# Kernel optimization log

Measured on AMD Instinct MI355X. Metric: run time of the kernel, lower is better.

Reference implementation:

```python
import jax, jax.numpy as jnp
import numpy as np
import math

D_MODEL = 128
NHEAD = 8


def setup_inputs() -> dict:
    key = jax.random.key(0)
    k1, k2 = jax.random.split(key)
    x = jax.random.normal(k1, (1, 128, 64, 64), dtype=jnp.float32)
    # Conv2d(in_c=128, out=3*d_model=384, kernel 1x1, bias=False) -> (384, 128)
    W_qkv = jax.random.normal(k2, (384, 128), dtype=jnp.float32) * (1.0 / math.sqrt(128))
    return {"x": x, "W_qkv": W_qkv}


def reference(x, W_qkv):
    b, c, h, w = x.shape
    n = h * w
    d_head = D_MODEL // NHEAD
    # 1x1 conv == channel-wise linear projection
    qkv = jnp.einsum('bchw,oc->bohw', x, W_qkv)          # (b, 3*d_model, h, w)
    # flatten(2).reshape(b, nhead, -1, h*w).permute(0,1,3,2)
    t = qkv.reshape(b, NHEAD, 3 * d_head, n)
    t = jnp.transpose(t, (0, 1, 3, 2))                   # (b, nhead, n, 3*d_head)
    q, k, v = jnp.split(t, 3, axis=-1)                   # each (b, nhead, n, d_head)
    # NOTE: original scales by sqrt(d_model), not sqrt(d_head)
    scale = 1.0 / math.sqrt(D_MODEL)
    scores = jnp.einsum('bhnd,bhmd->bhnm', q * scale, k)  # (b, nhead, n, n)
    attn = jax.nn.softmax(scores, axis=-1)
    out = jnp.einsum('bhnm,bhmd->bhnd', attn, v)         # (b, nhead, n, d_head)
    out = jnp.transpose(out, (0, 1, 3, 2)).reshape(b, D_MODEL, h, w)
    return out
```

## Files before the change

kernel.cpp:

```cpp
#include <hip/hip_runtime.h>
#include <hip/hip_bf16.h>


typedef __attribute__((ext_vector_type(4))) float    f32x4;
typedef __attribute__((ext_vector_type(8))) short    s16x8;
typedef __attribute__((ext_vector_type(4))) short    s16x4;
typedef __attribute__((ext_vector_type(8))) __bf16   bf16x8;
typedef __attribute__((ext_vector_type(4))) unsigned u32x4;

union FragAB { s16x8 s; bf16x8 b; u32x4 u; };

__device__ __forceinline__ short f2bf(float f) {
    unsigned u = __float_as_uint(f);
    u += 0x7fff + ((u >> 16) & 1);
    return (short)(u >> 16);
}

__device__ __forceinline__ unsigned pkbf(float a, float b) {
    float2 f2; f2.x = a; f2.y = b;
    __hip_bfloat162 h = __float22bfloat162_rn(f2);
    unsigned r;
    __builtin_memcpy(&r, &h, 4);
    return r;
}

#if __has_builtin(__builtin_amdgcn_exp2f)
  #define FASTEXP(x) __builtin_amdgcn_exp2f(x)
  #define QK_SCALE 0.12751744154070513f
#else
  #define FASTEXP(x) __expf(x)
  #define QK_SCALE 0.08838834764831845f
#endif

__global__ __launch_bounds__(256) void qkv_kernel(
    const float* __restrict__ x, const float* __restrict__ w,
    short* __restrict__ qT, short* __restrict__ kv)
{
    __shared__ __align__(16) short xT[4][16][136];
    const int wv   = threadIdx.x >> 6;
    const int lane = threadIdx.x & 63;
    const int colL = lane & 15, quad = lane >> 4;
    const int n0 = blockIdx.x * 64 + wv * 16;
    const int oq = blockIdx.y;

    #pragma unroll
    for (int rr = 0; rr < 4; ++rr) {
        int c  = rr * 32 + (lane >> 1);
        int nh = (lane & 1) * 8;
        f32x4 a = *(const f32x4*)&x[c * 4096 + n0 + nh];
        f32x4 b = *(const f32x4*)&x[c * 4096 + n0 + nh + 4];
        #pragma unroll
        for (int t = 0; t < 4; ++t) {
            xT[wv][nh + t][c]     = f2bf(a[t]);
            xT[wv][nh + 4 + t][c] = f2bf(b[t]);
        }
    }
    __syncthreads();

    FragAB xb[4];
    #pragma unroll
    for (int ks = 0; ks < 4; ++ks)
        xb[ks].s = *(const s16x8*)&xT[wv][colL][ks * 32 + quad * 8];

    const int T    = blockIdx.x;
    const int wloc = wv * 16 + colL;
    const int cc   = wloc >> 5;
    const int bb   = (wloc >> 4) & 1;
    const int qp   = (wloc >> 2) & 3;
    const int jj   = bb * 4 + (wloc & 3);

    #pragma unroll
    for (int i = 0; i < 6; ++i) {
        const int otg  = oq * 6 + i;
        const int ob   = otg * 16;
        const int h    = otg / 3;
        const int kind = otg % 3;
        f32x4 acc = {0.f, 0.f, 0.f, 0.f};
        #pragma unroll
        for (int ks = 0; ks < 4; ++ks) {
            f32x4 wa0 = *(const f32x4*)&w[(ob + colL) * 128 + ks * 32 + quad * 8];
            f32x4 wa1 = *(const f32x4*)&w[(ob + colL) * 128 + ks * 32 + quad * 8 + 4];
            FragAB wa;
            #pragma unroll
            for (int t = 0; t < 4; ++t) {
                wa.s[t]     = f2bf(wa0[t]);
                wa.s[t + 4] = f2bf(wa1[t]);
            }
            acc = __builtin_amdgcn_mfma_f32_16x16x32_bf16(wa.b, xb[ks].b, acc, 0, 0, 0);
        }
        if (kind == 0) {
            s16x4 pk;
            #pragma unroll
            for (int r = 0; r < 4; ++r) pk[r] = f2bf(acc[r] * QK_SCALE);
            *(s16x4*)&qT[(h * 4096 + n0 + colL) * 16 + quad * 4] = pk;
        } else if (kind == 1) {
            s16x4 pk;
            #pragma unroll
            for (int r = 0; r < 4; ++r) pk[r] = f2bf(acc[r]);
            *(s16x4*)&kv[(h * 64 + T) * 2048 + wloc * 16 + quad * 4] = pk;
        } else {
            #pragma unroll
            for (int r = 0; r < 4; ++r) {
                int d = quad * 4 + r;
                kv[(h * 64 + T) * 2048 + 1024 + d * 64 + cc * 32 + qp * 8 + jj] = f2bf(acc[r]);
            }
        }
    }
}

template<int SPLIT>
__global__ __launch_bounds__(256) void attn_kernel(
    const short* __restrict__ qT, const short* __restrict__ kv,
    float* __restrict__ Opart, float* __restrict__ lpart,
    float* __restrict__ out)
{
    const int wv   = threadIdx.x >> 6;
    const int lane = threadIdx.x & 63;
    const int colL = lane & 15, quad = lane >> 4;

    const int bx = blockIdx.x;
    int s, h, b;
    if (SPLIT > 1) { s = bx >> 7; h = (bx >> 4) & 7; b = bx & 15; }
    else           { s = 0;       h = bx >> 4;       b = bx & 15; }
    const int qbase = b * 256 + wv * 64;
    const int nkt = 64 / SPLIT;

    FragAB qfs[4];
    #pragma unroll
    for (int u = 0; u < 4; ++u) {
        qfs[u].s = 0;
        if (quad < 2)
            qfs[u].s = *(const s16x8*)&qT[(h * 4096 + qbase + u * 16 + colL) * 16 + quad * 8];
    }

    FragAB ones;
    #pragma unroll
    for (int j = 0; j < 8; ++j) ones.s[j] = (short)0x3F80;

    f32x4 o[4], ol[4];
    #pragma unroll
    for (int u = 0; u < 4; ++u) {
        o[u]  = (f32x4){0.f, 0.f, 0.f, 0.f};
        ol[u] = (f32x4){0.f, 0.f, 0.f, 0.f};
    }

    const int voffK = colL * 16 + quad * 8;
    const int voffV = 1024 + colL * 64 + quad * 8;

    const short* kvb = kv + (h * 64 + s * nkt) * 2048;

    #pragma unroll
    for (int kt = 0; kt < nkt; ++kt) {
        FragAB kf[4], vf[2];
        #pragma unroll
        for (int t = 0; t < 4; ++t)
            kf[t].s = *(const s16x8*)&kvb[voffK + t * 256];
        #pragma unroll
        for (int c = 0; c < 2; ++c)
            vf[c].s = *(const s16x8*)&kvb[voffV + c * 32];
        kvb += 2048;

        #pragma unroll
        for (int u = 0; u < 4; ++u) {
            f32x4 st[4];
            #pragma unroll
            for (int t = 0; t < 4; ++t) {
                f32x4 z = {0.f, 0.f, 0.f, 0.f};
                st[t] = __builtin_amdgcn_mfma_f32_16x16x32_bf16(kf[t].b, qfs[u].b, z, 0, 0, 0);
            }
            FragAB p0, p1;
            #pragma unroll
            for (int t = 0; t < 2; ++t) {
                p0.u[t * 2 + 0] = pkbf(FASTEXP(st[t][0]), FASTEXP(st[t][1]));
                p0.u[t * 2 + 1] = pkbf(FASTEXP(st[t][2]), FASTEXP(st[t][3]));
                p1.u[t * 2 + 0] = pkbf(FASTEXP(st[t + 2][0]), FASTEXP(st[t + 2][1]));
                p1.u[t * 2 + 1] = pkbf(FASTEXP(st[t + 2][2]), FASTEXP(st[t + 2][3]));
            }
            o[u]  = __builtin_amdgcn_mfma_f32_16x16x32_bf16(vf[0].b, p0.b, o[u],  0, 0, 0);
            ol[u] = __builtin_amdgcn_mfma_f32_16x16x32_bf16(ones.b,  p0.b, ol[u], 0, 0, 0);
            o[u]  = __builtin_amdgcn_mfma_f32_16x16x32_bf16(vf[1].b, p1.b, o[u],  0, 0, 0);
            ol[u] = __builtin_amdgcn_mfma_f32_16x16x32_bf16(ones.b,  p1.b, ol[u], 0, 0, 0);
        }
    }

    #pragma unroll
    for (int u = 0; u < 4; ++u) {
        const float l = ol[u][0];
        const int q0 = qbase + u * 16;
        if (SPLIT > 1) {
            #pragma unroll
            for (int r = 0; r < 4; ++r)
                Opart[((s * 8 + h) * 16 + quad * 4 + r) * 4096 + q0 + colL] = o[u][r];
            if (quad == 0) lpart[(s * 8 + h) * 4096 + q0 + colL] = l;
        } else {
            const float inv = 1.f / l;
            #pragma unroll
            for (int r = 0; r < 4; ++r)
                out[(h * 16 + quad * 4 + r) * 4096 + q0 + colL] = o[u][r] * inv;
        }
    }
}

template<int SPLIT>
__global__ __launch_bounds__(256) void combine_kernel(
    const float* __restrict__ Opart, const float* __restrict__ lpart,
    float* __restrict__ out)
{
    const int row = blockIdx.x >> 2;
    const int n   = (blockIdx.x & 3) * 1024 + threadIdx.x * 4;
    const int h   = row >> 4;
    f32x4 osum = {0.f, 0.f, 0.f, 0.f}, lsum = {0.f, 0.f, 0.f, 0.f};
    #pragma unroll
    for (int s = 0; s < SPLIT; ++s) {
        osum += *(const f32x4*)&Opart[(s * 128 + row) * 4096 + n];
        lsum += *(const f32x4*)&lpart[(s * 8 + h) * 4096 + n];
    }
    f32x4 res;
    #pragma unroll
    for (int r = 0; r < 4; ++r) res[r] = osum[r] / lsum[r];
    *(f32x4*)&out[row * 4096 + n] = res;
}

extern "C" void kernel_launch(void* const* d_in, const int* in_sizes, int n_in,
                              void* d_out, int out_size, void* d_ws, size_t ws_size,
                              hipStream_t stream) {
    const float* x = (const float*)d_in[0];
    const float* w = (const float*)d_in[1];
    float* out = (float*)d_out;

    char* ws = (char*)d_ws;
    short* qT = (short*)ws;
    short* kv = (short*)(ws + (1u << 20));

    constexpr int SPLIT = 8;
    const size_t opart_bytes = (size_t)SPLIT * 128 * 4096 * 4;
    const size_t lpart_bytes = (size_t)SPLIT * 8 * 4096 * 4;
    const size_t need_split  = (3ull << 20) + opart_bytes + lpart_bytes;

    dim3 gq(64, 4);
    qkv_kernel<<<gq, 256, 0, stream>>>(x, w, qT, kv);

    if (ws_size >= need_split) {
        float* Opart = (float*)(ws + (3ull << 20));
        float* lpart = (float*)(ws + (3ull << 20) + opart_bytes);
        attn_kernel<SPLIT><<<SPLIT * 128, 256, 0, stream>>>(qT, kv, Opart, lpart, out);
        combine_kernel<SPLIT><<<512, 256, 0, stream>>>(Opart, lpart, out);
    } else {
        attn_kernel<1><<<128, 256, 0, stream>>>(qT, kv, nullptr, nullptr, out);
    }
}
```

Before: 97.16 us.

## Split keys across waves in-block and combine via LDS, dropping combine kernel

Replaces the grid-level split-K attention, which wrote partial O and l to global memory and reduced them in a separate combine kernel, with 512-thread blocks. Each of the 8 waves in a block handles one eighth of the keys for the same 64 queries, and the partials are reduced through shared memory. This removes the global partial-result traffic and one kernel launch. It also uses the 16x16x16 bf16 MFMA for QK^T when available, so the 16-wide head dimension is no longer zero-padded to 32. The costs are a block-wide sync and higher register and LDS pressure per block.

Measured after the change: 86.37 us. -11.1%, faster.

```diff
diff --git a/kernel.cpp b/kernel.cpp
--- a/kernel.cpp
+++ b/kernel.cpp
@@ -30,6 +30,12 @@
 #else
   #define FASTEXP(x) __expf(x)
   #define QK_SCALE 0.08838834764831845f
+#endif
+
+#if __has_builtin(__builtin_amdgcn_mfma_f32_16x16x16bf16_1k)
+  #define HAVE_MFMA16 1
+#else
+  #define HAVE_MFMA16 0
 #endif
 
 __global__ __launch_bounds__(256) void qkv_kernel(
@@ -108,23 +114,27 @@
     }
 }
 
-template<int SPLIT>
-__global__ __launch_bounds__(256) void attn_kernel(
+__global__ __launch_bounds__(512, 4) void attn_kernel(
     const short* __restrict__ qT, const short* __restrict__ kv,
-    float* __restrict__ Opart, float* __restrict__ lpart,
     float* __restrict__ out)
 {
+    __shared__ float lds_o[8][16][66];
+    __shared__ float lds_l[8][64];
+
     const int wv   = threadIdx.x >> 6;
     const int lane = threadIdx.x & 63;
     const int colL = lane & 15, quad = lane >> 4;
 
-    const int bx = blockIdx.x;
-    int s, h, b;
-    if (SPLIT > 1) { s = bx >> 7; h = (bx >> 4) & 7; b = bx & 15; }
-    else           { s = 0;       h = bx >> 4;       b = bx & 15; }
-    const int qbase = b * 256 + wv * 64;
-    const int nkt = 64 / SPLIT;
-
+    const int h     = blockIdx.x >> 6;
+    const int qb    = blockIdx.x & 63;
+    const int qbase = qb * 64;
+
+#if HAVE_MFMA16
+    s16x4 qfs[4];
+    #pragma unroll
+    for (int u = 0; u < 4; ++u)
+        qfs[u] = *(const s16x4*)&qT[(h * 4096 + qbase + u * 16 + colL) * 16 + quad * 4];
+#else
     FragAB qfs[4];
     #pragma unroll
     for (int u = 0; u < 4; ++u) {
@@ -132,6 +142,7 @@
         if (quad < 2)
             qfs[u].s = *(const s16x8*)&qT[(h * 4096 + qbase + u * 16 + colL) * 16 + quad * 8];
     }
+#endif
 
     FragAB ones;
     #pragma unroll
@@ -144,17 +155,27 @@
         ol[u] = (f32x4){0.f, 0.f, 0.f, 0.f};
     }
 
-    const int voffK = colL * 16 + quad * 8;
-    const int voffV = 1024 + colL * 64 + quad * 8;
-
-    const short* kvb = kv + (h * 64 + s * nkt) * 2048;
-
-    #pragma unroll
-    for (int kt = 0; kt < nkt; ++kt) {
-        FragAB kf[4], vf[2];
+    const int voffK16 = colL * 16 + quad * 4;
+    const int voffK32 = colL * 16 + quad * 8;
+    const int voffV   = 1024 + colL * 64 + quad * 8;
+    (void)voffK32; (void)voffK16;
+
+    const short* kvb = kv + (h * 64 + wv * 8) * 2048;
+
+    #pragma unroll
+    for (int kt = 0; kt < 8; ++kt) {
+#if HAVE_MFMA16
+        s16x4 kf[4];
         #pragma unroll
         for (int t = 0; t < 4; ++t)
-            kf[t].s = *(const s16x8*)&kvb[voffK + t * 256];
+            kf[t] = *(const s16x4*)&kvb[voffK16 + t * 256];
+#else
+        FragAB kf[4];
+        #pragma unroll
+        for (int t = 0; t < 4; ++t)
+            kf[t].s = *(const s16x8*)&kvb[voffK32 + t * 256];
+#endif
+        FragAB vf[2];
         #pragma unroll
         for (int c = 0; c < 2; ++c)
             vf[c].s = *(const s16x8*)&kvb[voffV + c * 32];
@@ -166,7 +187,11 @@
             #pragma unroll
             for (int t = 0; t < 4; ++t) {
                 f32x4 z = {0.f, 0.f, 0.f, 0.f};
+#if HAVE_MFMA16
+                st[t] = __builtin_amdgcn_mfma_f32_16x16x16bf16_1k(kf[t], qfs[u], z, 0, 0, 0);
+#else
                 st[t] = __builtin_amdgcn_mfma_f32_16x16x32_bf16(kf[t].b, qfs[u].b, z, 0, 0, 0);
+#endif
             }
             FragAB p0, p1;
             #pragma unroll
@@ -185,40 +210,31 @@
 
     #pragma unroll
     for (int u = 0; u < 4; ++u) {
-        const float l = ol[u][0];
-        const int q0 = qbase + u * 16;
-        if (SPLIT > 1) {
-            #pragma unroll
-            for (int r = 0; r < 4; ++r)
-                Opart[((s * 8 + h) * 16 + quad * 4 + r) * 4096 + q0 + colL] = o[u][r];
-            if (quad == 0) lpart[(s * 8 + h) * 4096 + q0 + colL] = l;
-        } else {
-            const float inv = 1.f / l;
-            #pragma unroll
-            for (int r = 0; r < 4; ++r)
-                out[(h * 16 + quad * 4 + r) * 4096 + q0 + colL] = o[u][r] * inv;
-        }
-    }
-}
-
-template<int SPLIT>
-__global__ __launch_bounds__(256) void combine_kernel(
-    const float* __restrict__ Opart, const float* __restrict__ lpart,
-    float* __restrict__ out)
-{
-    const int row = blockIdx.x >> 2;
-    const int n   = (blockIdx.x & 3) * 1024 + threadIdx.x * 4;
-    const int h   = row >> 4;
-    f32x4 osum = {0.f, 0.f, 0.f, 0.f}, lsum = {0.f, 0.f, 0.f, 0.f};
-    #pragma unroll
-    for (int s = 0; s < SPLIT; ++s) {
-        osum += *(const f32x4*)&Opart[(s * 128 + row) * 4096 + n];
-        lsum += *(const f32x4*)&lpart[(s * 8 + h) * 4096 + n];
-    }
-    f32x4 res;
-    #pragma unroll
-    for (int r = 0; r < 4; ++r) res[r] = osum[r] / lsum[r];
-    *(f32x4*)&out[row * 4096 + n] = res;
+        #pragma unroll
+        for (int r = 0; r < 4; ++r)
+            lds_o[wv][quad * 4 + r][u * 16 + colL] = o[u][r];
+    }
+    if (quad == 0) {
+        #pragma unroll
+        for (int u = 0; u < 4; ++u)
+            lds_l[wv][u * 16 + colL] = ol[u][0];
+    }
+    __syncthreads();
+
+    const int d  = threadIdx.x >> 5;
+    const int q2 = (threadIdx.x & 31) * 2;
+    float ox = 0.f, oy = 0.f, lx = 0.f, ly = 0.f;
+    #pragma unroll
+    for (int s = 0; s < 8; ++s) {
+        float2 ov = *(const float2*)&lds_o[s][d][q2];
+        float2 lv = *(const float2*)&lds_l[s][q2];
+        ox += ov.x; oy += ov.y;
+        lx += lv.x; ly += lv.y;
+    }
+    float2 res;
+    res.x = ox / lx;
+    res.y = oy / ly;
+    *(float2*)&out[(h * 16 + d) * 4096 + qbase + q2] = res;
 }
 
 extern "C" void kernel_launch(void* const* d_in, const int* in_sizes, int n_in,
@@ -232,20 +248,7 @@
     short* qT = (short*)ws;
     short* kv = (short*)(ws + (1u << 20));
 
-    constexpr int SPLIT = 8;
-    const size_t opart_bytes = (size_t)SPLIT * 128 * 4096 * 4;
-    const size_t lpart_bytes = (size_t)SPLIT * 8 * 4096 * 4;
-    const size_t need_split  = (3ull << 20) + opart_bytes + lpart_bytes;
-
     dim3 gq(64, 4);
     qkv_kernel<<<gq, 256, 0, stream>>>(x, w, qT, kv);
-
-    if (ws_size >= need_split) {
-        float* Opart = (float*)(ws + (3ull << 20));
-        float* lpart = (float*)(ws + (3ull << 20) + opart_bytes);
-        attn_kernel<SPLIT><<<SPLIT * 128, 256, 0, stream>>>(qT, kv, Opart, lpart, out);
-        combine_kernel<SPLIT><<<512, 256, 0, stream>>>(Opart, lpart, out);
-    } else {
-        attn_kernel<1><<<128, 256, 0, stream>>>(qT, kv, nullptr, nullptr, out);
-    }
-}
+    attn_kernel<<<512, 512, 0, stream>>>(qT, kv, out);
+}
```
